# Optimization experiments

Measured on AMD Instinct MI355X. Metric: run time of the kernel, lower is better.

The kernel has to match this reference:

```python
import jax, jax.numpy as jnp
import numpy as np

RADII = (0.8, 1.6)
NSAMPLES = (16, 32)
IN_C = 64
BN_EPS = 1e-3  # BN1d eps; eval-mode BN with running stats (0, 1)
B, N_PER, M_PER = 2, 8192, 2048
BOX = (40.0, 40.0, 4.0)  # point cloud extent in meters


def _batch_ids(cnt, total):
    # point i belongs to batch searchsorted(cumsum(cnt), i, 'right')
    return jnp.searchsorted(jnp.cumsum(cnt), jnp.arange(total), side='right')


def _ball_group(xyz, bid, new_xyz, nbid, feats, radius, nsample):
    # Ball query (stacked-batch): first `nsample` points within `radius` of each
    # query, same batch only; pad short balls with the first found index;
    # fully-empty balls are zeroed (pcdet QueryAndGroup semantics).
    d2 = jnp.sum((new_xyz[:, None, :] - xyz[None, :, :]) ** 2, axis=-1)  # (M, N)
    within = (d2 < radius * radius) & (nbid[:, None] == bid[None, :])
    n = xyz.shape[0]
    score = jnp.where(within, -jnp.arange(n, dtype=jnp.float32), -jnp.inf)
    vals, idx = jax.lax.top_k(score, nsample)  # smallest in-ball indices first
    valid = jnp.isfinite(vals)
    idx = jnp.where(valid, idx, idx[:, :1])  # pad with first found index
    empty = ~valid[:, :1]  # (M, 1): no point in ball
    g_xyz = xyz[idx] - new_xyz[:, None, :]          # (M, ns, 3) relative coords
    g = jnp.concatenate([g_xyz, feats[idx]], -1)    # (M, ns, 3 + C), xyz first
    return jnp.where(empty[:, :, None], 0.0, g)


def _shared_mlp(x, layers):
    # Conv1d(k=1, bias=False) + BN1d(eval, mean=0, var=1) + ReLU per layer
    inv_std = 1.0 / jnp.sqrt(1.0 + BN_EPS)
    for w, g, b in layers:
        x = jnp.einsum('mnc,oc->mno', x, w)
        x = jax.nn.relu(x * (g * inv_std) + b)
    return x  # (M, ns, cout)


def setup_inputs() -> dict:
    key = jax.random.key(0)
    ks = jax.random.split(key, 16)
    box = jnp.asarray(BOX, dtype=jnp.float32)
    xyz = jax.random.uniform(ks[0], (B * N_PER, 3), dtype=jnp.float32) * box
    new_xyz = jax.random.uniform(ks[1], (B * M_PER, 3), dtype=jnp.float32) * box
    features = jax.random.normal(ks[2], (B * N_PER, IN_C), dtype=jnp.float32)

    def conv_w(k, cin, cout):
        return jax.random.normal(k, (cout, cin), dtype=jnp.float32) / np.sqrt(cin)

    cin = IN_C + 3  # use_xyz -> +3
    inp = dict(xyz=xyz, features=features, new_xyz=new_xyz,
               w00=conv_w(ks[3], cin, 64), g00=jnp.ones(64), b00=jnp.zeros(64),
               w01=conv_w(ks[4], 64, 64), g01=jnp.ones(64), b01=jnp.zeros(64),
               w10=conv_w(ks[5], cin, 64), g10=jnp.ones(64), b10=jnp.zeros(64),
               w11=conv_w(ks[6], 64, 64), g11=jnp.ones(64), b11=jnp.zeros(64),
               xyz_batch_cnt=jnp.full((B,), N_PER, dtype=jnp.int32),
               new_xyz_batch_cnt=jnp.full((B,), M_PER, dtype=jnp.int32))
    return inp


def reference(xyz, features, new_xyz,
              w00, g00, b00, w01, g01, b01,
              w10, g10, b10, w11, g11, b11,
              xyz_batch_cnt, new_xyz_batch_cnt):
    bid = _batch_ids(xyz_batch_cnt, xyz.shape[0])
    nbid = _batch_ids(new_xyz_batch_cnt, new_xyz.shape[0])
    layer_params = [[(w00, g00, b00), (w01, g01, b01)],
                    [(w10, g10, b10), (w11, g11, b11)]]
    outs = []
    for k in range(len(RADII)):
        g = _ball_group(xyz, bid, new_xyz, nbid, features, RADII[k], NSAMPLES[k])
        h = _shared_mlp(g, layer_params[k])
        outs.append(jnp.max(h, axis=1))  # max-pool over neighbors
    return jnp.concatenate(outs, axis=1)  # (M_tot, 128)
```

## Files before the change

### kernel.cpp

```cpp
#include <hip/hip_runtime.h>
#include <hip/hip_bf16.h>
#include <stdint.h>


#define NS0 16
#define NS1 32
#define NXC 25
#define NYC 25
#define NZC 3
#define CPB (NXC * NYC * NZC)
#define CINV 0.625f
#define CSZ 1.6f
#define CAP 48

typedef _Float16 half8 __attribute__((ext_vector_type(8)));
typedef float f32x4 __attribute__((ext_vector_type(4)));

static __device__ __forceinline__ half8 cvt8(float4 a, float4 b) {
    half8 r;
    r[0] = (_Float16)a.x; r[1] = (_Float16)a.y; r[2] = (_Float16)a.z; r[3] = (_Float16)a.w;
    r[4] = (_Float16)b.x; r[5] = (_Float16)b.y; r[6] = (_Float16)b.z; r[7] = (_Float16)b.w;
    return r;
}
static __device__ __forceinline__ uint32_t pk2(float x, float y) {
    const _Float16 a = (_Float16)x, c = (_Float16)y;
    return (uint32_t)__builtin_bit_cast(uint16_t, a) |
           ((uint32_t)__builtin_bit_cast(uint16_t, c) << 16);
}

__global__ __launch_bounds__(256) void prep(
    const float* __restrict__ w00, const float* __restrict__ g00, const float* __restrict__ b00,
    const float* __restrict__ w01, const float* __restrict__ g01, const float* __restrict__ b01,
    const float* __restrict__ w10, const float* __restrict__ g10, const float* __restrict__ b10,
    const float* __restrict__ w11, const float* __restrict__ g11, const float* __restrict__ b11,
    float* __restrict__ wpk, int* __restrict__ cell_cnt, int n4)
{
    if (blockIdx.x >= 2) {
        const int i = (blockIdx.x - 2) * 256 + threadIdx.x;
        if (i < n4) ((int4*)cell_cnt)[i] = make_int4(0, 0, 0, 0);
        return;
    }
    const int k = blockIdx.x;
    const int tid = threadIdx.x;
    const int lane = tid & 63, t = tid >> 6;
    const int p = lane & 15, h = lane >> 4;
    const float* W1 = k ? w10 : w00; const float* G1 = k ? g10 : g00; const float* B1 = k ? b10 : b00;
    const float* W2 = k ? w11 : w01; const float* G2 = k ? g11 : g01; const float* B2 = k ? b11 : b01;
    const float inv = 1.0f / sqrtf(1.0f + 1e-3f);

    uint32_t* outw = (uint32_t*)wpk + (size_t)k * 6144;
    const int m = 16 * t + p;
    const float sc1 = G1[m] * inv;
    #pragma unroll
    for (int s = 0; s < 3; ++s) {
        #pragma unroll
        for (int r = 0; r < 4; ++r) {
            uint32_t u = 0;
            #pragma unroll
            for (int e = 0; e < 2; ++e) {
                const int cpad = 32 * s + 8 * h + 2 * r + e;
                float val = 0.f;
                if (cpad < 64)       val = W1[m * 67 + 3 + cpad] * sc1;
                else if (cpad < 67)  val = W1[m * 67 + (cpad - 64)] * sc1;
                else if (cpad == 67) val = B1[m];
                const _Float16 hv = (_Float16)val;
                u |= ((uint32_t)__builtin_bit_cast(uint16_t, hv)) << (16 * e);
            }
            outw[((t * 3 + s) * 64 + lane) * 4 + r] = u;
        }
    }
    const float sc2 = G2[m] * inv;
    uint32_t* outw2 = outw + 3072;
    #pragma unroll
    for (int s = 0; s < 2; ++s) {
        #pragma unroll
        for (int r = 0; r < 4; ++r) {
            uint32_t u = 0;
            #pragma unroll
            for (int e = 0; e < 2; ++e) {
                const int cch = 32 * s + 8 * h + 2 * r + e;
                const _Float16 hv = (_Float16)(W2[m * 64 + cch] * sc2);
                u |= ((uint32_t)__builtin_bit_cast(uint16_t, hv)) << (16 * e);
            }
            outw2[((t * 2 + s) * 64 + lane) * 4 + r] = u;
        }
    }
    float* bo = wpk + (size_t)k * 6144 + 5120;
    #pragma unroll
    for (int r = 0; r < 4; ++r)
        bo[(t * 64 + lane) * 4 + r] = B2[16 * t + 4 * h + r];
}

__global__ __launch_bounds__(256) void bin_cap(
    const float* __restrict__ xyz, const int* __restrict__ xcnt, int B, int N,
    int* __restrict__ cell_cnt, float4* __restrict__ binned4)
{
    const int i = blockIdx.x * 256 + threadIdx.x;
    if (i >= N) return;
    int acc = 0, b = 0;
    for (int k = 0; k < B; ++k) { int c = xcnt[k]; if (i >= acc && i < acc + c) b = k; acc += c; }
    const float x = xyz[3 * i], y = xyz[3 * i + 1], z = xyz[3 * i + 2];
    const int cx = min(NXC - 1, max(0, (int)floorf(x * CINV)));
    const int cy = min(NYC - 1, max(0, (int)floorf(y * CINV)));
    const int cz = min(NZC - 1, max(0, (int)floorf(z * CINV)));
    const int cell = b * CPB + (cz * NYC + cy) * NXC + cx;
    const int slot = atomicAdd(&cell_cnt[cell], 1);
    if (slot < CAP) {
        float4 r; r.x = x; r.y = y; r.z = z; r.w = __int_as_float(i);
        binned4[(size_t)cell * CAP + slot] = r;
    }
}

static __device__ __forceinline__ void mlp_one(
    int c_pts, int ntmax, float4 eA, float4 eB,
    const uint4* __restrict__ wlds, char* __restrict__ hb,
    const float* __restrict__ feats, const float4* __restrict__ bq,
    float* __restrict__ out_base, bool qvalid, int lane)
{
    const int p = lane & 15, h = lane >> 4;
    const int nt = min((c_pts + 15) >> 4, ntmax);

    f32x4 macc[4] = {f32x4(-3e38f), f32x4(-3e38f), f32x4(-3e38f), f32x4(-3e38f)};

    half8 b0a[2], b1a[2], b2a[2];
    bool ona[2];
    #pragma unroll
    for (int pt = 0; pt < 2; ++pt) {
        b0a[pt] = 0; b1a[pt] = 0; b2a[pt] = 0; ona[pt] = false;
        if (pt < nt) {
            const int gp = pt * 16 + p;
            const bool on = gp < c_pts;
            ona[pt] = on;
            if (on) {
                const float4 e = pt ? eB : eA;
                const int j = (int)(__float_as_uint(e.w) >> 1);
                const float4* f0p = (const float4*)(feats + (size_t)j * 64 + 8 * h);
                const float4* f1p = (const float4*)(feats + (size_t)j * 64 + 32 + 8 * h);
                b0a[pt] = cvt8(f0p[0], f0p[1]);
                b1a[pt] = cvt8(f1p[0], f1p[1]);
                if (h == 0) {
                    half8 b2 = 0;
                    b2[0] = (_Float16)e.x;
                    b2[1] = (_Float16)e.y;
                    b2[2] = (_Float16)e.z;
                    b2[3] = (_Float16)1.0f;
                    b2a[pt] = b2;
                }
            }
        }
    }

    #pragma unroll
    for (int pt = 0; pt < 2; ++pt) {
        if (pt < nt) {
            f32x4 acc[4] = {f32x4(0.f), f32x4(0.f), f32x4(0.f), f32x4(0.f)};
            #pragma unroll
            for (int t = 0; t < 4; ++t) {
                #pragma unroll
                for (int s = 0; s < 3; ++s) {
                    const half8 a = __builtin_bit_cast(half8, wlds[(t * 3 + s) * 64 + lane]);
                    const half8 bf = (s == 0) ? b0a[pt] : ((s == 1) ? b1a[pt] : b2a[pt]);
                    acc[t] = __builtin_amdgcn_mfma_f32_16x16x32_f16(a, bf, acc[t], 0, 0, 0);
                }
            }
            #pragma unroll
            for (int t = 0; t < 4; ++t) {
                *(uint32_t*)(hb + 144 * p + 32 * t + 8 * h) =
                    pk2(fmaxf(acc[t][0], 0.f), fmaxf(acc[t][1], 0.f));
                *(uint32_t*)(hb + 144 * p + 32 * t + 8 * h + 4) =
                    pk2(fmaxf(acc[t][2], 0.f), fmaxf(acc[t][3], 0.f));
            }
            const half8 g0 = *(const half8*)(hb + 144 * p + 16 * h);
            const half8 g1 = *(const half8*)(hb + 144 * p + 64 + 16 * h);

            f32x4 acc2[4] = {f32x4(0.f), f32x4(0.f), f32x4(0.f), f32x4(0.f)};
            #pragma unroll
            for (int t = 0; t < 4; ++t) {
                #pragma unroll
                for (int s = 0; s < 2; ++s) {
                    const half8 a = __builtin_bit_cast(half8, wlds[768 + (t * 2 + s) * 64 + lane]);
                    const half8 bf = (s == 0) ? g0 : g1;
                    acc2[t] = __builtin_amdgcn_mfma_f32_16x16x32_f16(a, bf, acc2[t], 0, 0, 0);
                }
            }
            #pragma unroll
            for (int t = 0; t < 4; ++t)
                #pragma unroll
                for (int r = 0; r < 4; ++r)
                    if (ona[pt]) macc[t][r] = fmaxf(macc[t][r], acc2[t][r]);
        }
    }

    #pragma unroll
    for (int d = 1; d < 16; d <<= 1)
        #pragma unroll
        for (int t = 0; t < 4; ++t)
            #pragma unroll
            for (int r = 0; r < 4; ++r)
                macc[t][r] = fmaxf(macc[t][r], __shfl_xor(macc[t][r], d));

    if (p == 0 && qvalid) {
        float* o = out_base + 4 * h;
        #pragma unroll
        for (int t = 0; t < 4; ++t) {
            const float4 bb = bq[t * 64 + lane];
            float4 v;
            v.x = fmaxf(macc[t][0] + bb.x, 0.f);
            v.y = fmaxf(macc[t][1] + bb.y, 0.f);
            v.z = fmaxf(macc[t][2] + bb.z, 0.f);
            v.w = fmaxf(macc[t][3] + bb.w, 0.f);
            *(float4*)(o + 16 * t) = v;
        }
    }
}

__global__ __launch_bounds__(256, 4) void query_mlp(
    const float* __restrict__ feats,
    const float* __restrict__ new_xyz, const int* __restrict__ ncnt,
    const int* __restrict__ cell_cnt, const float4* __restrict__ binned4,
    const float* __restrict__ wpk, int B, int M,
    float* __restrict__ out)
{
    __shared__ uint4 wlds[1280];
    __shared__ float4 uni[4][176];

    const int tid = threadIdx.x;
    const int wave = tid >> 6, lane = tid & 63;
    const int gw = blockIdx.x * 4 + wave;
    const bool qvalid = gw < M;
    const int m = qvalid ? gw : 0;
    const int p = lane & 15;

    {
        const uint4* ws = (const uint4*)((const uint32_t*)wpk);
        #pragma unroll
        for (int i = 0; i < 5; ++i) wlds[tid + 256 * i] = ws[tid + 256 * i];
    }

    int cA = 0, cB = 0;
    float4 ek0, ek1a, ek1b;
    {
        int acc = 0, b = 0;
        for (int k2 = 0; k2 < B; ++k2) { int c = ncnt[k2]; if (m >= acc && m < acc + c) b = k2; acc += c; }
        const float qx = new_xyz[3 * m], qy = new_xyz[3 * m + 1], qz = new_xyz[3 * m + 2];
        const float R0S = 0.64f, R1S = 2.56f;
        const float PAD = 1.60002f;

        const int lx = max(0, (int)floorf((qx - PAD) * CINV));
        const int hx = min(NXC - 1, (int)floorf((qx + PAD) * CINV));
        const int ly = max(0, (int)floorf((qy - PAD) * CINV));
        const int hy = min(NYC - 1, (int)floorf((qy + PAD) * CINV));
        const int lz = max(0, (int)floorf((qz - PAD) * CINV));
        const int hz = min(NZC - 1, (int)floorf((qz + PAD) * CINV));
        const int wx = hx - lx + 1, wy = hy - ly + 1, wz = hz - lz + 1;
        const int nw = wx * wy * wz;

        int cnt_l = 0, cell_l = 0;
        if (lane < nw) {
            const int wxy = wx * wy;
            const int ldz = lane / wxy;
            const int rem = lane - ldz * wxy;
            const int ldy = rem / wx;
            const int ldx = rem - ldy * wx;
            const int cx = lx + ldx, cy = ly + ldy, cz = lz + ldz;
            const float bx0 = cx * CSZ, by0 = cy * CSZ, bz0 = cz * CSZ;
            const float dx = (qx < bx0) ? (bx0 - qx) : ((qx > bx0 + CSZ) ? (qx - bx0 - CSZ) : 0.f);
            const float dy = (qy < by0) ? (by0 - qy) : ((qy > by0 + CSZ) ? (qy - by0 - CSZ) : 0.f);
            const float dz = (qz < bz0) ? (bz0 - qz) : ((qz > bz0 + CSZ) ? (qz - bz0 - CSZ) : 0.f);
            const float md2 = dx * dx + dy * dy + dz * dz;
            cell_l = b * CPB + (cz * NYC + cy) * NXC + cx;
            if (md2 <= R1S + 1e-3f) cnt_l = min(cell_cnt[cell_l], CAP);
        }

        int incl = cnt_l;
        #pragma unroll
        for (int d = 1; d < 64; d <<= 1) {
            const int v = __shfl_up(incl, d);
            if (lane >= d) incl += v;
        }
        const int excl = incl - cnt_l;
        const int tot = __shfl(incl, 63);

        float4* cd4 = &uni[wave][0];
        const unsigned long long lower = (lane == 0) ? 0ull : (~0ull >> (64 - lane));
        int c = 0, c0n = 0;

        for (int t0 = 0; t0 < tot; t0 += 64) {
            const int t = t0 + lane;
            const bool v = t < tot;
            int lo = 0, hi = 63;
            #pragma unroll
            for (int s = 0; s < 6; ++s) {
                const int mid = (lo + hi) >> 1;
                const int vm = __shfl(incl, mid);
                if (vm > t) hi = mid; else lo = mid + 1;
            }
            const int j = lo & 63;
            const int slot = t - __shfl(excl, j);
            const int cell = __shfl(cell_l, j);
            float d2 = 1e30f;
            float dx = 0.f, dy = 0.f, dzp = 0.f;
            int pid = 0;
            if (v) {
                const float4 e = binned4[(size_t)cell * CAP + slot];
                pid = __float_as_int(e.w);
                dx = e.x - qx; dy = e.y - qy; dzp = e.z - qz;
                d2 = __fadd_rn(__fadd_rn(__fmul_rn(dx, dx), __fmul_rn(dy, dy)),
                               __fmul_rn(dzp, dzp));
            }
            const bool keep = v && (d2 < R1S);
            const bool f0 = keep && (d2 < R0S);
            const unsigned long long mk = __ballot(keep);
            if (keep) {
                const int pos = c + __popcll(mk & lower);
                if (pos < 128) {
                    const uint32_t key = ((uint32_t)pid << 1) | (f0 ? 1u : 0u);
                    cd4[pos] = make_float4(dx, dy, dzp, __uint_as_float(key));
                }
            }
            c += __popcll(mk);
            c0n += __popcll(__ballot(f0));
        }

        const int cc = min(c, 128);
        float4* L4a = &uni[wave][128];
        float4* L4b = &uni[wave][144];
        const float4 fa = (lane < cc) ? cd4[lane]
                                      : make_float4(0, 0, 0, __uint_as_float(0xFFFFFFFFu));
        const float4 fb = (64 + lane < cc) ? cd4[64 + lane]
                                           : make_float4(0, 0, 0, __uint_as_float(0xFFFFFFFFu));
        const uint32_t ka = __float_as_uint(fa.w), kb = __float_as_uint(fb.w);
        int ra = 0, ra0 = 0, rb = 0, rb0 = 0;
        for (int e2 = 0; e2 < cc; e2 += 4) {
            #pragma unroll
            for (int u = 0; u < 4; ++u) {
                const int ee = e2 + u;
                if (ee < cc) {
                    const uint32_t ke = __float_as_uint(cd4[ee].w);
                    const int sm_a = (ke < ka), sm_b = (ke < kb), f = (int)(ke & 1u);
                    ra += sm_a; ra0 += sm_a & f;
                    rb += sm_b; rb0 += sm_b & f;
                }
            }
        }
        if (lane < cc) {
            if ((ka & 1u) && ra0 < NS0) L4a[ra0] = fa;
            if (ra < NS1) L4b[ra] = fa;
        }
        if (64 + lane < cc) {
            if ((kb & 1u) && rb0 < NS0) L4a[rb0] = fb;
            if (rb < NS1) L4b[rb] = fb;
        }
        cA = min(c0n, NS0);
        cB = min(c, NS1);

        ek0  = L4a[p];
        ek1a = L4b[p];
        ek1b = L4b[16 + p];
    }

    __syncthreads();

    char* hb = (char*)&uni[wave][0];
    mlp_one(cA, 1, ek0, ek0, wlds, hb, feats,
            (const float4*)(wpk + 5120), out + (size_t)m * 128, qvalid, lane);

    __syncthreads();

    {
        const uint4* ws = (const uint4*)((const uint32_t*)wpk + 6144);
        #pragma unroll
        for (int i = 0; i < 5; ++i) wlds[tid + 256 * i] = ws[tid + 256 * i];
    }
    __syncthreads();

    mlp_one(cB, 2, ek1a, ek1b, wlds, hb, feats,
            (const float4*)(wpk + 6144 + 5120), out + (size_t)m * 128 + 64,
            qvalid, lane);
}

extern "C" void kernel_launch(void* const* d_in, const int* in_sizes, int n_in,
                              void* d_out, int out_size, void* d_ws, size_t ws_size,
                              hipStream_t stream) {
    const float* xyz     = (const float*)d_in[0];
    const float* feats   = (const float*)d_in[1];
    const float* new_xyz = (const float*)d_in[2];
    const float* w00 = (const float*)d_in[3];
    const float* g00 = (const float*)d_in[4];
    const float* b00 = (const float*)d_in[5];
    const float* w01 = (const float*)d_in[6];
    const float* g01 = (const float*)d_in[7];
    const float* b01 = (const float*)d_in[8];
    const float* w10 = (const float*)d_in[9];
    const float* g10 = (const float*)d_in[10];
    const float* b10 = (const float*)d_in[11];
    const float* w11 = (const float*)d_in[12];
    const float* g11 = (const float*)d_in[13];
    const float* b11 = (const float*)d_in[14];
    const int* xcnt = (const int*)d_in[15];
    const int* ncnt = (const int*)d_in[16];

    const int B = in_sizes[15];
    const int N = in_sizes[0] / 3;
    const int M = in_sizes[2] / 3;
    const int ncells = B * CPB;
    const int ncells_pad = (ncells + 3) & ~3;

    uint32_t* w32 = (uint32_t*)d_ws;
    float* wpk      = (float*)w32;
    int* cell_cnt   = (int*)(w32 + 12288);
    float4* binned4 = (float4*)(cell_cnt + ncells_pad);

    const int n4 = ncells_pad >> 2;
    const int zero_blocks = (n4 + 255) / 256;
    prep<<<2 + zero_blocks, 256, 0, stream>>>(
        w00, g00, b00, w01, g01, b01, w10, g10, b10, w11, g11, b11,
        wpk, cell_cnt, n4);
    bin_cap<<<(N + 255) / 256, 256, 0, stream>>>(xyz, xcnt, B, N,
                                                 cell_cnt, binned4);
    query_mlp<<<(M + 3) / 4, 256, 0, stream>>>(feats, new_xyz, ncnt,
                                               cell_cnt, binned4, wpk, B, M,
                                               (float*)d_out);
}
```

Before: 32.83 us.

## Drop prep kernel: bin per-batch with LDS histogram and pack weights in-kernel

Removes the separate weight-prep/zeroing kernel. Binning now runs one 1024-thread block per batch, with cell counts held in a shared-memory histogram that is written out at the end. Each query block converts and packs the fp32 weights to fp16 directly into LDS, and reads the second-layer bias from global. This cuts one kernel launch and the global atomics, at the cost of running binning on only B blocks and repeating weight conversion in every query block.

Result: slower. 35.64 us (+8.6%).

```diff
diff --git a/kernel.cpp b/kernel.cpp
--- a/kernel.cpp
+++ b/kernel.cpp
@@ -28,27 +28,46 @@
            ((uint32_t)__builtin_bit_cast(uint16_t, c) << 16);
 }
 
-__global__ __launch_bounds__(256) void prep(
-    const float* __restrict__ w00, const float* __restrict__ g00, const float* __restrict__ b00,
-    const float* __restrict__ w01, const float* __restrict__ g01, const float* __restrict__ b01,
-    const float* __restrict__ w10, const float* __restrict__ g10, const float* __restrict__ b10,
-    const float* __restrict__ w11, const float* __restrict__ g11, const float* __restrict__ b11,
-    float* __restrict__ wpk, int* __restrict__ cell_cnt, int n4)
+__global__ __launch_bounds__(1024) void bin2(
+    const float* __restrict__ xyz, const int* __restrict__ xcnt, int B, int N,
+    int* __restrict__ cell_cnt, float4* __restrict__ binned4)
 {
-    if (blockIdx.x >= 2) {
-        const int i = (blockIdx.x - 2) * 256 + threadIdx.x;
-        if (i < n4) ((int4*)cell_cnt)[i] = make_int4(0, 0, 0, 0);
-        return;
-    }
-    const int k = blockIdx.x;
+    __shared__ int hist[CPB];
+    const int b = blockIdx.x;
     const int tid = threadIdx.x;
+
+    int xs = 0;
+    for (int k = 0; k < b; ++k) xs += xcnt[k];
+    const int xe = xs + xcnt[b];
+
+    for (int c = tid; c < CPB; c += 1024) hist[c] = 0;
+    __syncthreads();
+
+    for (int i = xs + tid; i < xe; i += 1024) {
+        const float x = xyz[3 * i], y = xyz[3 * i + 1], z = xyz[3 * i + 2];
+        const int cx = min(NXC - 1, max(0, (int)floorf(x * CINV)));
+        const int cy = min(NYC - 1, max(0, (int)floorf(y * CINV)));
+        const int cz = min(NZC - 1, max(0, (int)floorf(z * CINV)));
+        const int cell = (cz * NYC + cy) * NXC + cx;
+        const int slot = atomicAdd(&hist[cell], 1);
+        if (slot < CAP) {
+            float4 r; r.x = x; r.y = y; r.z = z; r.w = __int_as_float(i);
+            binned4[((size_t)(b * CPB + cell)) * CAP + slot] = r;
+        }
+    }
+    __syncthreads();
+
+    for (int c = tid; c < CPB; c += 1024) cell_cnt[b * CPB + c] = hist[c];
+}
+
+static __device__ __forceinline__ void pack_wlds(
+    uint32_t* __restrict__ wl, int tid,
+    const float* __restrict__ W1, const float* __restrict__ G1, const float* __restrict__ B1,
+    const float* __restrict__ W2, const float* __restrict__ G2)
+{
     const int lane = tid & 63, t = tid >> 6;
     const int p = lane & 15, h = lane >> 4;
-    const float* W1 = k ? w10 : w00; const float* G1 = k ? g10 : g00; const float* B1 = k ? b10 : b00;
-    const float* W2 = k ? w11 : w01; const float* G2 = k ? g11 : g01; const float* B2 = k ? b11 : b01;
     const float inv = 1.0f / sqrtf(1.0f + 1e-3f);
-
-    uint32_t* outw = (uint32_t*)wpk + (size_t)k * 6144;
     const int m = 16 * t + p;
     const float sc1 = G1[m] * inv;
     #pragma unroll
@@ -66,11 +85,10 @@
                 const _Float16 hv = (_Float16)val;
                 u |= ((uint32_t)__builtin_bit_cast(uint16_t, hv)) << (16 * e);
             }
-            outw[((t * 3 + s) * 64 + lane) * 4 + r] = u;
+            wl[((t * 3 + s) * 64 + lane) * 4 + r] = u;
         }
     }
     const float sc2 = G2[m] * inv;
-    uint32_t* outw2 = outw + 3072;
     #pragma unroll
     for (int s = 0; s < 2; ++s) {
         #pragma unroll
@@ -82,39 +100,15 @@
                 const _Float16 hv = (_Float16)(W2[m * 64 + cch] * sc2);
                 u |= ((uint32_t)__builtin_bit_cast(uint16_t, hv)) << (16 * e);
             }
-            outw2[((t * 2 + s) * 64 + lane) * 4 + r] = u;
-        }
-    }
-    float* bo = wpk + (size_t)k * 6144 + 5120;
-    #pragma unroll
-    for (int r = 0; r < 4; ++r)
-        bo[(t * 64 + lane) * 4 + r] = B2[16 * t + 4 * h + r];
-}
-
-__global__ __launch_bounds__(256) void bin_cap(
-    const float* __restrict__ xyz, const int* __restrict__ xcnt, int B, int N,
-    int* __restrict__ cell_cnt, float4* __restrict__ binned4)
-{
-    const int i = blockIdx.x * 256 + threadIdx.x;
-    if (i >= N) return;
-    int acc = 0, b = 0;
-    for (int k = 0; k < B; ++k) { int c = xcnt[k]; if (i >= acc && i < acc + c) b = k; acc += c; }
-    const float x = xyz[3 * i], y = xyz[3 * i + 1], z = xyz[3 * i + 2];
-    const int cx = min(NXC - 1, max(0, (int)floorf(x * CINV)));
-    const int cy = min(NYC - 1, max(0, (int)floorf(y * CINV)));
-    const int cz = min(NZC - 1, max(0, (int)floorf(z * CINV)));
-    const int cell = b * CPB + (cz * NYC + cy) * NXC + cx;
-    const int slot = atomicAdd(&cell_cnt[cell], 1);
-    if (slot < CAP) {
-        float4 r; r.x = x; r.y = y; r.z = z; r.w = __int_as_float(i);
-        binned4[(size_t)cell * CAP + slot] = r;
+            wl[3072 + ((t * 2 + s) * 64 + lane) * 4 + r] = u;
+        }
     }
 }
 
 static __device__ __forceinline__ void mlp_one(
     int c_pts, int ntmax, float4 eA, float4 eB,
     const uint4* __restrict__ wlds, char* __restrict__ hb,
-    const float* __restrict__ feats, const float4* __restrict__ bq,
+    const float* __restrict__ feats, const float* __restrict__ B2,
     float* __restrict__ out_base, bool qvalid, int lane)
 {
     const int p = lane & 15, h = lane >> 4;
@@ -203,7 +197,7 @@
         float* o = out_base + 4 * h;
         #pragma unroll
         for (int t = 0; t < 4; ++t) {
-            const float4 bb = bq[t * 64 + lane];
+            const float4 bb = *(const float4*)(B2 + 16 * t + 4 * h);
             float4 v;
             v.x = fmaxf(macc[t][0] + bb.x, 0.f);
             v.y = fmaxf(macc[t][1] + bb.y, 0.f);
@@ -218,8 +212,11 @@
     const float* __restrict__ feats,
     const float* __restrict__ new_xyz, const int* __restrict__ ncnt,
     const int* __restrict__ cell_cnt, const float4* __restrict__ binned4,
-    const float* __restrict__ wpk, int B, int M,
-    float* __restrict__ out)
+    const float* __restrict__ w00, const float* __restrict__ g00, const float* __restrict__ b00,
+    const float* __restrict__ w01, const float* __restrict__ g01, const float* __restrict__ b01,
+    const float* __restrict__ w10, const float* __restrict__ g10, const float* __restrict__ b10,
+    const float* __restrict__ w11, const float* __restrict__ g11, const float* __restrict__ b11,
+    int B, int M, float* __restrict__ out)
 {
     __shared__ uint4 wlds[1280];
     __shared__ float4 uni[4][176];
@@ -231,11 +228,7 @@
     const int m = qvalid ? gw : 0;
     const int p = lane & 15;
 
-    {
-        const uint4* ws = (const uint4*)((const uint32_t*)wpk);
-        #pragma unroll
-        for (int i = 0; i < 5; ++i) wlds[tid + 256 * i] = ws[tid + 256 * i];
-    }
+    pack_wlds((uint32_t*)wlds, tid, w00, g00, b00, w01, g01);
 
     int cA = 0, cB = 0;
     float4 ek0, ek1a, ek1b;
@@ -362,21 +355,16 @@
     __syncthreads();
 
     char* hb = (char*)&uni[wave][0];
-    mlp_one(cA, 1, ek0, ek0, wlds, hb, feats,
-            (const float4*)(wpk + 5120), out + (size_t)m * 128, qvalid, lane);
+    mlp_one(cA, 1, ek0, ek0, wlds, hb, feats, b01,
+            out + (size_t)m * 128, qvalid, lane);
 
     __syncthreads();
 
-    {
-        const uint4* ws = (const uint4*)((const uint32_t*)wpk + 6144);
-        #pragma unroll
-        for (int i = 0; i < 5; ++i) wlds[tid + 256 * i] = ws[tid + 256 * i];
-    }
+    pack_wlds((uint32_t*)wlds, tid, w10, g10, b10, w11, g11);
     __syncthreads();
 
-    mlp_one(cB, 2, ek1a, ek1b, wlds, hb, feats,
-            (const float4*)(wpk + 6144 + 5120), out + (size_t)m * 128 + 64,
-            qvalid, lane);
+    mlp_one(cB, 2, ek1a, ek1b, wlds, hb, feats, b11,
+            out + (size_t)m * 128 + 64, qvalid, lane);
 }
 
 extern "C" void kernel_launch(void* const* d_in, const int* in_sizes, int n_in,
@@ -407,18 +395,12 @@
     const int ncells_pad = (ncells + 3) & ~3;
 
     uint32_t* w32 = (uint32_t*)d_ws;
-    float* wpk      = (float*)w32;
-    int* cell_cnt   = (int*)(w32 + 12288);
-    float4* binned4 = (float4*)(cell_cnt + ncells_pad);
-
-    const int n4 = ncells_pad >> 2;
-    const int zero_blocks = (n4 + 255) / 256;
-    prep<<<2 + zero_blocks, 256, 0, stream>>>(
+    int* cell_cnt   = (int*)w32;
+    float4* binned4 = (float4*)(w32 + ncells_pad);
+
+    bin2<<<B, 1024, 0, stream>>>(xyz, xcnt, B, N, cell_cnt, binned4);
+    query_mlp<<<(M + 3) / 4, 256, 0, stream>>>(
+        feats, new_xyz, ncnt, cell_cnt, binned4,
         w00, g00, b00, w01, g01, b01, w10, g10, b10, w11, g11, b11,
-        wpk, cell_cnt, n4);
-    bin_cap<<<(N + 255) / 256, 256, 0, stream>>>(xyz, xcnt, B, N,
-                                                 cell_cnt, binned4);
-    query_mlp<<<(M + 3) / 4, 256, 0, stream>>>(feats, new_xyz, ncnt,
-                                               cell_cnt, binned4, wpk, B, M,
-                                               (float*)d_out);
-}
+        B, M, (float*)d_out);
+}
```

## Fuse weight prep and spatial binning into one kernel with per-batch LDS histograms

Applied to the files above, without the earlier changes.

Merges the weight-packing, cell-count zeroing and point-binning kernels into a single launch. Each batch gets one 1024-thread block that bins its points with LDS atomics and then writes the counts out, so the separate zeroing pass and the global atomics go away. This saves a kernel launch and global atomic traffic, but binning 8192 points now runs on only one block per batch, which limits parallelism.

Result: faster. 31.95 us (-2.7%).

```diff
diff --git a/kernel.cpp b/kernel.cpp
--- a/kernel.cpp
+++ b/kernel.cpp
@@ -28,87 +28,95 @@
            ((uint32_t)__builtin_bit_cast(uint16_t, c) << 16);
 }
 
-__global__ __launch_bounds__(256) void prep(
+__global__ __launch_bounds__(1024) void prep_bin(
+    const float* __restrict__ xyz, const int* __restrict__ xcnt, int N,
     const float* __restrict__ w00, const float* __restrict__ g00, const float* __restrict__ b00,
     const float* __restrict__ w01, const float* __restrict__ g01, const float* __restrict__ b01,
     const float* __restrict__ w10, const float* __restrict__ g10, const float* __restrict__ b10,
     const float* __restrict__ w11, const float* __restrict__ g11, const float* __restrict__ b11,
-    float* __restrict__ wpk, int* __restrict__ cell_cnt, int n4)
+    float* __restrict__ wpk, int* __restrict__ cell_cnt,
+    float4* __restrict__ binned4)
 {
-    if (blockIdx.x >= 2) {
-        const int i = (blockIdx.x - 2) * 256 + threadIdx.x;
-        if (i < n4) ((int4*)cell_cnt)[i] = make_int4(0, 0, 0, 0);
+    if (blockIdx.x < 2) {
+        const int k = blockIdx.x;
+        const int tid = threadIdx.x;
+        if (tid >= 256) return;
+        const int lane = tid & 63, t = tid >> 6;
+        const int p = lane & 15, h = lane >> 4;
+        const float* W1 = k ? w10 : w00; const float* G1 = k ? g10 : g00; const float* B1 = k ? b10 : b00;
+        const float* W2 = k ? w11 : w01; const float* G2 = k ? g11 : g01; const float* B2 = k ? b11 : b01;
+        const float inv = 1.0f / sqrtf(1.0f + 1e-3f);
+
+        uint32_t* outw = (uint32_t*)wpk + (size_t)k * 6144;
+        const int m = 16 * t + p;
+        const float sc1 = G1[m] * inv;
+        #pragma unroll
+        for (int s = 0; s < 3; ++s) {
+            #pragma unroll
+            for (int r = 0; r < 4; ++r) {
+                uint32_t u = 0;
+                #pragma unroll
+                for (int e = 0; e < 2; ++e) {
+                    const int cpad = 32 * s + 8 * h + 2 * r + e;
+                    float val = 0.f;
+                    if (cpad < 64)       val = W1[m * 67 + 3 + cpad] * sc1;
+                    else if (cpad < 67)  val = W1[m * 67 + (cpad - 64)] * sc1;
+                    else if (cpad == 67) val = B1[m];
+                    const _Float16 hv = (_Float16)val;
+                    u |= ((uint32_t)__builtin_bit_cast(uint16_t, hv)) << (16 * e);
+                }
+                outw[((t * 3 + s) * 64 + lane) * 4 + r] = u;
+            }
+        }
+        const float sc2 = G2[m] * inv;
+        uint32_t* outw2 = outw + 3072;
+        #pragma unroll
+        for (int s = 0; s < 2; ++s) {
+            #pragma unroll
+            for (int r = 0; r < 4; ++r) {
+                uint32_t u = 0;
+                #pragma unroll
+                for (int e = 0; e < 2; ++e) {
+                    const int cch = 32 * s + 8 * h + 2 * r + e;
+                    const _Float16 hv = (_Float16)(W2[m * 64 + cch] * sc2);
+                    u |= ((uint32_t)__builtin_bit_cast(uint16_t, hv)) << (16 * e);
+                }
+                outw2[((t * 2 + s) * 64 + lane) * 4 + r] = u;
+            }
+        }
+        float* bo = wpk + (size_t)k * 6144 + 5120;
+        #pragma unroll
+        for (int r = 0; r < 4; ++r)
+            bo[(t * 64 + lane) * 4 + r] = B2[16 * t + 4 * h + r];
         return;
     }
-    const int k = blockIdx.x;
+
+    __shared__ int hist[CPB];
+    const int b = blockIdx.x - 2;
     const int tid = threadIdx.x;
-    const int lane = tid & 63, t = tid >> 6;
-    const int p = lane & 15, h = lane >> 4;
-    const float* W1 = k ? w10 : w00; const float* G1 = k ? g10 : g00; const float* B1 = k ? b10 : b00;
-    const float* W2 = k ? w11 : w01; const float* G2 = k ? g11 : g01; const float* B2 = k ? b11 : b01;
-    const float inv = 1.0f / sqrtf(1.0f + 1e-3f);
-
-    uint32_t* outw = (uint32_t*)wpk + (size_t)k * 6144;
-    const int m = 16 * t + p;
-    const float sc1 = G1[m] * inv;
-    #pragma unroll
-    for (int s = 0; s < 3; ++s) {
-        #pragma unroll
-        for (int r = 0; r < 4; ++r) {
-            uint32_t u = 0;
-            #pragma unroll
-            for (int e = 0; e < 2; ++e) {
-                const int cpad = 32 * s + 8 * h + 2 * r + e;
-                float val = 0.f;
-                if (cpad < 64)       val = W1[m * 67 + 3 + cpad] * sc1;
-                else if (cpad < 67)  val = W1[m * 67 + (cpad - 64)] * sc1;
-                else if (cpad == 67) val = B1[m];
-                const _Float16 hv = (_Float16)val;
-                u |= ((uint32_t)__builtin_bit_cast(uint16_t, hv)) << (16 * e);
-            }
-            outw[((t * 3 + s) * 64 + lane) * 4 + r] = u;
-        }
-    }
-    const float sc2 = G2[m] * inv;
-    uint32_t* outw2 = outw + 3072;
-    #pragma unroll
-    for (int s = 0; s < 2; ++s) {
-        #pragma unroll
-        for (int r = 0; r < 4; ++r) {
-            uint32_t u = 0;
-            #pragma unroll
-            for (int e = 0; e < 2; ++e) {
-                const int cch = 32 * s + 8 * h + 2 * r + e;
-                const _Float16 hv = (_Float16)(W2[m * 64 + cch] * sc2);
-                u |= ((uint32_t)__builtin_bit_cast(uint16_t, hv)) << (16 * e);
-            }
-            outw2[((t * 2 + s) * 64 + lane) * 4 + r] = u;
-        }
-    }
-    float* bo = wpk + (size_t)k * 6144 + 5120;
-    #pragma unroll
-    for (int r = 0; r < 4; ++r)
-        bo[(t * 64 + lane) * 4 + r] = B2[16 * t + 4 * h + r];
-}
-
-__global__ __launch_bounds__(256) void bin_cap(
-    const float* __restrict__ xyz, const int* __restrict__ xcnt, int B, int N,
-    int* __restrict__ cell_cnt, float4* __restrict__ binned4)
-{
-    const int i = blockIdx.x * 256 + threadIdx.x;
-    if (i >= N) return;
-    int acc = 0, b = 0;
-    for (int k = 0; k < B; ++k) { int c = xcnt[k]; if (i >= acc && i < acc + c) b = k; acc += c; }
-    const float x = xyz[3 * i], y = xyz[3 * i + 1], z = xyz[3 * i + 2];
-    const int cx = min(NXC - 1, max(0, (int)floorf(x * CINV)));
-    const int cy = min(NYC - 1, max(0, (int)floorf(y * CINV)));
-    const int cz = min(NZC - 1, max(0, (int)floorf(z * CINV)));
-    const int cell = b * CPB + (cz * NYC + cy) * NXC + cx;
-    const int slot = atomicAdd(&cell_cnt[cell], 1);
-    if (slot < CAP) {
-        float4 r; r.x = x; r.y = y; r.z = z; r.w = __int_as_float(i);
-        binned4[(size_t)cell * CAP + slot] = r;
-    }
+
+    int xs = 0;
+    for (int k = 0; k < b; ++k) xs += xcnt[k];
+    const int xe = xs + xcnt[b];
+
+    for (int c = tid; c < CPB; c += 1024) hist[c] = 0;
+    __syncthreads();
+
+    for (int i = xs + tid; i < xe; i += 1024) {
+        const float x = xyz[3 * i], y = xyz[3 * i + 1], z = xyz[3 * i + 2];
+        const int cx = min(NXC - 1, max(0, (int)floorf(x * CINV)));
+        const int cy = min(NYC - 1, max(0, (int)floorf(y * CINV)));
+        const int cz = min(NZC - 1, max(0, (int)floorf(z * CINV)));
+        const int cell = (cz * NYC + cy) * NXC + cx;
+        const int slot = atomicAdd(&hist[cell], 1);
+        if (slot < CAP) {
+            float4 r; r.x = x; r.y = y; r.z = z; r.w = __int_as_float(i);
+            binned4[((size_t)(b * CPB + cell)) * CAP + slot] = r;
+        }
+    }
+    __syncthreads();
+
+    for (int c = tid; c < CPB; c += 1024) cell_cnt[b * CPB + c] = hist[c];
 }
 
 static __device__ __forceinline__ void mlp_one(
@@ -411,13 +419,10 @@
     int* cell_cnt   = (int*)(w32 + 12288);
     float4* binned4 = (float4*)(cell_cnt + ncells_pad);
 
-    const int n4 = ncells_pad >> 2;
-    const int zero_blocks = (n4 + 255) / 256;
-    prep<<<2 + zero_blocks, 256, 0, stream>>>(
+    prep_bin<<<2 + B, 1024, 0, stream>>>(
+        xyz, xcnt, N,
         w00, g00, b00, w01, g01, b01, w10, g10, b10, w11, g11, b11,
-        wpk, cell_cnt, n4);
-    bin_cap<<<(N + 255) / 256, 256, 0, stream>>>(xyz, xcnt, B, N,
-                                                 cell_cnt, binned4);
+        wpk, cell_cnt, binned4);
     query_mlp<<<(M + 3) / 4, 256, 0, stream>>>(feats, new_xyz, ncnt,
                                                cell_cnt, binned4, wpk, B, M,
                                                (float*)d_out);
```
